# Optimization experiments

Hardware: AMD Instinct MI355X
Metric: run time of the kernel (lower is better)

## Reference

```python
import jax, jax.numpy as jnp
import numpy as np

GRID_SIZE = 5
SPLINE_ORDER = 3

def _grid(in_features, dtype):
    # efficient-KAN default grid over [-1, 1], extended by spline_order knots each side
    h = 2.0 / GRID_SIZE
    g = jnp.arange(-SPLINE_ORDER, GRID_SIZE + SPLINE_ORDER + 1, dtype=dtype) * h - 1.0
    return jnp.broadcast_to(g, (in_features, g.shape[0]))  # (in, G+2k+1)

def _b_splines(x, grid):
    # x: (..., in) -> bases: (..., in, G+k) via Cox-de Boor recursion
    xk = x[..., None]
    bases = ((xk >= grid[:, :-1]) & (xk < grid[:, 1:])).astype(x.dtype)
    for k in range(1, SPLINE_ORDER + 1):
        left = (xk - grid[:, :-(k + 1)]) / (grid[:, k:-1] - grid[:, :-(k + 1)]) * bases[..., :-1]
        right = (grid[:, k + 1:] - xk) / (grid[:, k + 1:] - grid[:, 1:-k]) * bases[..., 1:]
        bases = left + right
    return bases

def _kan_linear(x, base_w, spline_w, scaler):
    # base branch: SiLU(x) @ W_base^T ; spline branch: einsum over B-spline basis
    grid = _grid(base_w.shape[1], x.dtype)
    bases = _b_splines(x, grid)                      # (..., in, G+k)
    scaled = spline_w * scaler[..., None]            # (out, in, G+k)
    base_out = jax.nn.silu(x) @ base_w.T
    spline_out = jnp.einsum('...ig,oig->...o', bases, scaled)
    return base_out + spline_out

def setup_inputs() -> dict:
    key = jax.random.key(0)
    ks = jax.random.split(key, 11)
    B, N, C, O = 2, 256, 64, 64
    GK = GRID_SIZE + SPLINE_ORDER
    return {
        'x': jax.random.normal(ks[0], (B, N, C), jnp.float32),
        'adj': jax.random.randint(ks[1], (B, N, N), 0, 2, jnp.int32),
        'fw_base': jax.random.normal(ks[2], (1, C), jnp.float32) * 0.1,
        'fw_spline': jax.random.normal(ks[3], (1, C, GK), jnp.float32) * 0.1,
        'fw_scaler': jax.random.normal(ks[4], (1, C), jnp.float32) * 0.1,
        'mw_base': jax.random.normal(ks[5], (O, C), jnp.float32) * 0.1,
        'mw_spline': jax.random.normal(ks[6], (O, C, GK), jnp.float32) * 0.1,
        'mw_scaler': jax.random.normal(ks[7], (O, C), jnp.float32) * 0.1,
        'uw_base': jax.random.normal(ks[8], (O, C + O), jnp.float32) * 0.1,
        'uw_spline': jax.random.normal(ks[9], (O, C + O, GK), jnp.float32) * 0.1,
        'uw_scaler': jax.random.normal(ks[10], (O, C + O), jnp.float32) * 0.1,
    }

def reference(x, adj, fw_base, fw_spline, fw_scaler, mw_base, mw_spline, mw_scaler, uw_base, uw_spline, uw_scaler):
    # r_ij = h_i - h_j : (B, N, N, C)
    r_ij = x[:, :, None, :] - x[:, None, :, :]
    energy = _kan_linear(r_ij, fw_base, fw_spline, fw_scaler)[..., 0]  # (B, N, N)
    energy = jnp.where(adj == 0, jnp.asarray(-1e9, energy.dtype), energy)
    alpha = jax.nn.softmax(energy, axis=-1)
    msg_val = _kan_linear(x, mw_base, mw_spline, mw_scaler)            # (B, N, O)
    aggr = jnp.einsum('bij,bjo->bio', alpha, msg_val)
    combined = jnp.concatenate([x, aggr], axis=-1)
    return _kan_linear(combined, uw_base, uw_spline, uw_scaler)
```

## Files before the change

### kernel.cpp

```cpp
#include <hip/hip_runtime.h>
#include <math.h>

#define NB 256
#define CH 64
#define OUTF 64
#define GK 8
#define UIN 128
#define KM (CH * 9)
#define KM4 (KM / 4)
#define KU (UIN * 9)
#define KU4 (KU / 4)

#define WS_MSG 0
#define WS_XT 32768
#define WS_W2M 65536
#define WS_W2U 102400

__device__ __forceinline__ float silu(float v) {
    return v * __builtin_amdgcn_rcpf(1.0f + __expf(-v));
}

__device__ __forceinline__ void spline4(float r, int& d, float4& v) {
    float p = (r + 2.2f) * 2.5f;
    float fd = floorf(p);
    d = (int)fd;
    float u = p - fd;
    if ((unsigned)d > 10u) d = 11;
    float um = 1.0f - u;
    float u2 = u * u, u3 = u2 * u;
    const float k6 = 1.0f / 6.0f;
    v.x = um * um * um * k6;
    v.y = (3.0f * u3 - 6.0f * u2 + 4.0f) * k6;
    v.z = (-3.0f * u3 + 3.0f * u2 + 3.0f * u + 1.0f) * k6;
    v.w = u3 * k6;
}

__global__ __launch_bounds__(256) void prep_kernel(
    const float* __restrict__ x,
    const float* __restrict__ mwb, const float* __restrict__ mws,
    const float* __restrict__ mwsc,
    const float* __restrict__ uwb, const float* __restrict__ uws,
    const float* __restrict__ uwsc,
    float* __restrict__ ws) {
    int t = blockIdx.x * 256 + threadIdx.x;
    if (t < 2 * NB * CH) {
        int b = t >> 14, rem = t & 16383, j = rem >> 6, c = rem & 63;
        ws[WS_XT + b * CH * NB + c * NB + j] = x[t];
        return;
    }
    int t2 = t - 2 * NB * CH;
    if (t2 < KM4 * OUTF) {
        int k4 = t2 >> 6, o = t2 & 63;
        float4 v;
#pragma unroll
        for (int kk = 0; kk < 4; ++kk) {
            int k = k4 * 4 + kk, c = k / 9, g = k - c * 9;
            ((float*)&v)[kk] = (g < 8)
                ? mws[(o * CH + c) * GK + g] * mwsc[o * CH + c]
                : mwb[o * CH + c];
        }
        ((float4*)(ws + WS_W2M))[t2] = v;
        return;
    }
    int t3 = t2 - KM4 * OUTF;
    if (t3 < KU4 * OUTF) {
        int k4 = t3 >> 6, o = t3 & 63;
        float4 v;
#pragma unroll
        for (int kk = 0; kk < 4; ++kk) {
            int k = k4 * 4 + kk, c = k / 9, g = k - c * 9;
            ((float*)&v)[kk] = (g < 8)
                ? uws[(o * UIN + c) * GK + g] * uwsc[o * UIN + c]
                : uwb[o * UIN + c];
        }
        ((float4*)(ws + WS_W2U))[t3] = v;
    }
}

__global__ __launch_bounds__(256) void msg_kernel(
    const float* __restrict__ x, const float* __restrict__ w2m,
    float* __restrict__ msg) {
    const int row = blockIdx.x, tid = threadIdx.x;
    __shared__ __align__(16) float F[KM];
    __shared__ float part[4][OUTF];

    if (tid < CH) {
        float v = x[row * CH + tid];
#pragma unroll
        for (int g = 0; g < 8; ++g) F[tid * 9 + g] = 0.0f;
        F[tid * 9 + 8] = silu(v);
        int d; float4 vv; spline4(v, d, vv);
#pragma unroll
        for (int k = 0; k < 4; ++k) {
            int m = d - 3 + k;
            if ((unsigned)m < 8u) F[tid * 9 + m] = ((const float*)&vv)[k];
        }
    }
    __syncthreads();

    const int o = tid & 63, w = tid >> 6;
    const float4* W = (const float4*)w2m;
    const float4* Fv = (const float4*)F;
    float acc = 0.0f;
#pragma unroll 4
    for (int k4 = w * 36; k4 < w * 36 + 36; ++k4) {
        float4 f = Fv[k4];
        float4 wt = W[k4 * 64 + o];
        acc += f.x * wt.x + f.y * wt.y + f.z * wt.z + f.w * wt.w;
    }
    part[w][o] = acc;
    __syncthreads();
    if (tid < OUTF)
        msg[row * OUTF + tid] =
            part[0][tid] + part[1][tid] + part[2][tid] + part[3][tid];
}

__global__ __launch_bounds__(256) void gat_kernel(
    const float* __restrict__ xT,
    const float* __restrict__ x,
    const int* __restrict__ adj,
    const float* __restrict__ fwb, const float* __restrict__ fws,
    const float* __restrict__ fwsc,
    const float* __restrict__ w2u,
    const float* __restrict__ msg,
    float* __restrict__ out) {
    const int b = blockIdx.x >> 8;
    const int i = blockIdx.x & 255;
    const int tid = threadIdx.x;

    __shared__ float4 cpad[CH][16];
    __shared__ float2 xisf[CH];
    __shared__ float alpha[NB];
    __shared__ float comb[UIN];
    __shared__ __align__(16) float Fu[KU];
    __shared__ float part[4][OUTF];
    __shared__ float wred[4];

    if (tid < CH) {
        float v = x[(b * NB + i) * CH + tid];
        xisf[tid] = make_float2(v, fwb[tid]);
        comb[tid] = v;
    }
#pragma unroll
    for (int e = tid; e < CH * 16; e += 256) {
        int c = e >> 4, dd = e & 15;
        float4 cf = make_float4(0.f, 0.f, 0.f, 0.f);
        if (dd <= 10) {
            float sc = fwsc[c];
            float w0 = 0.f, w1 = 0.f, w2 = 0.f, w3 = 0.f;
            int m0 = dd - 3;
            if ((unsigned)(m0 + 0) < 8u) w0 = fws[c * GK + m0 + 0] * sc;
            if ((unsigned)(m0 + 1) < 8u) w1 = fws[c * GK + m0 + 1] * sc;
            if ((unsigned)(m0 + 2) < 8u) w2 = fws[c * GK + m0 + 2] * sc;
            if ((unsigned)(m0 + 3) < 8u) w3 = fws[c * GK + m0 + 3] * sc;
            cf.x = (w0 + 4.0f * w1 + w2) * (1.0f / 6.0f);
            cf.y = (w2 - w0) * 0.5f;
            cf.z = (w0 - 2.0f * w1 + w2) * 0.5f;
            cf.w = (w3 - w0 + 3.0f * (w1 - w2)) * (1.0f / 6.0f);
        }
        cpad[c][dd] = cf;
    }
    __syncthreads();

    const float* xTb = xT + b * CH * NB;
    float e = 0.0f;
#pragma unroll 4
    for (int c = 0; c < CH; ++c) {
        float xj = xTb[c * NB + tid];
        float2 xs = xisf[c];
        float r = xs.x - xj;
        float pp = (r + 2.2f) * 2.5f;
        float fd = floorf(pp);
        int d = (int)fd;
        float u = pp - fd;
        if ((unsigned)d > 10u) d = 11;
        float4 cf = cpad[c][d];
        e += cf.x + u * (cf.y + u * (cf.z + u * cf.w)) + silu(r) * xs.y;
    }
    if (adj[(b * NB + i) * NB + tid] == 0) e = -1e9f;

    float mx = e;
#pragma unroll
    for (int off = 32; off > 0; off >>= 1)
        mx = fmaxf(mx, __shfl_xor(mx, off, 64));
    if ((tid & 63) == 0) wred[tid >> 6] = mx;
    __syncthreads();
    mx = fmaxf(fmaxf(wred[0], wred[1]), fmaxf(wred[2], wred[3]));
    float pexp = __expf(e - mx);
    float sw = pexp;
#pragma unroll
    for (int off = 32; off > 0; off >>= 1)
        sw += __shfl_xor(sw, off, 64);
    __syncthreads();
    if ((tid & 63) == 0) wred[tid >> 6] = sw;
    __syncthreads();
    float denom = wred[0] + wred[1] + wred[2] + wred[3];
    alpha[tid] = pexp * __builtin_amdgcn_rcpf(denom);
    __syncthreads();

    {
        const int o = tid & 63, seg = tid >> 6;
        const float* msgb = msg + (b * NB + seg * 64) * OUTF;
        float a = 0.0f;
#pragma unroll 8
        for (int jj = 0; jj < 64; ++jj)
            a += alpha[seg * 64 + jj] * msgb[jj * OUTF + o];
        part[seg][o] = a;
    }
    __syncthreads();
    if (tid < OUTF)
        comb[CH + tid] = part[0][tid] + part[1][tid] + part[2][tid] + part[3][tid];
    __syncthreads();

    if (tid < UIN) {
        float v = comb[tid];
#pragma unroll
        for (int g = 0; g < 8; ++g) Fu[tid * 9 + g] = 0.0f;
        Fu[tid * 9 + 8] = silu(v);
        int d; float4 vv; spline4(v, d, vv);
#pragma unroll
        for (int k = 0; k < 4; ++k) {
            int m = d - 3 + k;
            if ((unsigned)m < 8u) Fu[tid * 9 + m] = ((const float*)&vv)[k];
        }
    }
    __syncthreads();

    {
        const int o = tid & 63, w = tid >> 6;
        const float4* W = (const float4*)w2u;
        const float4* Fv = (const float4*)Fu;
        float acc = 0.0f;
#pragma unroll 4
        for (int k4 = w * 72; k4 < w * 72 + 72; ++k4) {
            float4 f = Fv[k4];
            float4 wt = W[k4 * 64 + o];
            acc += f.x * wt.x + f.y * wt.y + f.z * wt.z + f.w * wt.w;
        }
        part[w][o] = acc;
    }
    __syncthreads();
    if (tid < OUTF)
        out[(b * NB + i) * OUTF + tid] =
            part[0][tid] + part[1][tid] + part[2][tid] + part[3][tid];
}

extern "C" void kernel_launch(void* const* d_in, const int* in_sizes, int n_in,
                              void* d_out, int out_size, void* d_ws, size_t ws_size,
                              hipStream_t stream) {
    const float* x     = (const float*)d_in[0];
    const int*   adj   = (const int*)d_in[1];
    const float* fwb   = (const float*)d_in[2];
    const float* fws   = (const float*)d_in[3];
    const float* fwsc  = (const float*)d_in[4];
    const float* mwb   = (const float*)d_in[5];
    const float* mws   = (const float*)d_in[6];
    const float* mwsc  = (const float*)d_in[7];
    const float* uwb   = (const float*)d_in[8];
    const float* uws   = (const float*)d_in[9];
    const float* uwsc  = (const float*)d_in[10];
    float* out = (float*)d_out;
    float* ws = (float*)d_ws;

    const int BN = in_sizes[0] / CH;

    const int prep_threads = 2 * NB * CH + KM4 * OUTF + KU4 * OUTF;
    prep_kernel<<<(prep_threads + 255) / 256, 256, 0, stream>>>(
        x, mwb, mws, mwsc, uwb, uws, uwsc, ws);
    msg_kernel<<<BN, 256, 0, stream>>>(x, ws + WS_W2M, ws + WS_MSG);
    gat_kernel<<<BN, 256, 0, stream>>>(ws + WS_XT, x, adj, fwb, fws, fwsc,
                                       ws + WS_W2U, ws + WS_MSG, out);
}
```

Baseline: 100.8 us.

## Load x_j rows into registers, drop transpose, vectorize alpha-msg aggregation

Removes the transpose of x in the prep kernel. In the gat kernel, each thread now loads its own row of x (64 floats as float4) into registers, where it previously read the transposed copy column by column. The pairwise energy loop is fully unrolled with fma-based polynomial evaluation. The alpha·msg aggregation switches to float4 loads across 16 segments, and launch bounds hint two blocks per CU. The 64-float register array raises register pressure, and the per-thread row loads are strided rather than coalesced.

New measurement: 99.39 us. Within noise of the previous version (-1.4%).

```diff
diff --git a/kernel.cpp b/kernel.cpp
--- a/kernel.cpp
+++ b/kernel.cpp
@@ -12,16 +12,15 @@
 #define KU4 (KU / 4)
 
 #define WS_MSG 0
-#define WS_XT 32768
-#define WS_W2M 65536
-#define WS_W2U 102400
+#define WS_W2M 32768
+#define WS_W2U 69632
 
 __device__ __forceinline__ float silu(float v) {
     return v * __builtin_amdgcn_rcpf(1.0f + __expf(-v));
 }
 
 __device__ __forceinline__ void spline4(float r, int& d, float4& v) {
-    float p = (r + 2.2f) * 2.5f;
+    float p = fmaf(r, 2.5f, 5.5f);
     float fd = floorf(p);
     d = (int)fd;
     float u = p - fd;
@@ -36,21 +35,14 @@
 }
 
 __global__ __launch_bounds__(256) void prep_kernel(
-    const float* __restrict__ x,
     const float* __restrict__ mwb, const float* __restrict__ mws,
     const float* __restrict__ mwsc,
     const float* __restrict__ uwb, const float* __restrict__ uws,
     const float* __restrict__ uwsc,
     float* __restrict__ ws) {
     int t = blockIdx.x * 256 + threadIdx.x;
-    if (t < 2 * NB * CH) {
-        int b = t >> 14, rem = t & 16383, j = rem >> 6, c = rem & 63;
-        ws[WS_XT + b * CH * NB + c * NB + j] = x[t];
-        return;
-    }
-    int t2 = t - 2 * NB * CH;
-    if (t2 < KM4 * OUTF) {
-        int k4 = t2 >> 6, o = t2 & 63;
+    if (t < KM4 * OUTF) {
+        int k4 = t >> 6, o = t & 63;
         float4 v;
 #pragma unroll
         for (int kk = 0; kk < 4; ++kk) {
@@ -59,12 +51,12 @@
                 ? mws[(o * CH + c) * GK + g] * mwsc[o * CH + c]
                 : mwb[o * CH + c];
         }
-        ((float4*)(ws + WS_W2M))[t2] = v;
+        ((float4*)(ws + WS_W2M))[t] = v;
         return;
     }
-    int t3 = t2 - KM4 * OUTF;
-    if (t3 < KU4 * OUTF) {
-        int k4 = t3 >> 6, o = t3 & 63;
+    int t2 = t - KM4 * OUTF;
+    if (t2 < KU4 * OUTF) {
+        int k4 = t2 >> 6, o = t2 & 63;
         float4 v;
 #pragma unroll
         for (int kk = 0; kk < 4; ++kk) {
@@ -73,7 +65,7 @@
                 ? uws[(o * UIN + c) * GK + g] * uwsc[o * UIN + c]
                 : uwb[o * UIN + c];
         }
-        ((float4*)(ws + WS_W2U))[t3] = v;
+        ((float4*)(ws + WS_W2U))[t2] = v;
     }
 }
 
@@ -115,8 +107,7 @@
             part[0][tid] + part[1][tid] + part[2][tid] + part[3][tid];
 }
 
-__global__ __launch_bounds__(256) void gat_kernel(
-    const float* __restrict__ xT,
+__global__ __launch_bounds__(256, 2) void gat_kernel(
     const float* __restrict__ x,
     const int* __restrict__ adj,
     const float* __restrict__ fwb, const float* __restrict__ fws,
@@ -129,17 +120,27 @@
     const int tid = threadIdx.x;
 
     __shared__ float4 cpad[CH][16];
-    __shared__ float2 xisf[CH];
+    __shared__ float4 xi4[16];
+    __shared__ float4 fb4[16];
     __shared__ float alpha[NB];
     __shared__ float comb[UIN];
     __shared__ __align__(16) float Fu[KU];
+    __shared__ float4 part4[16][16];
     __shared__ float part[4][OUTF];
     __shared__ float wred[4];
 
-    if (tid < CH) {
-        float v = x[(b * NB + i) * CH + tid];
-        xisf[tid] = make_float2(v, fwb[tid]);
-        comb[tid] = v;
+    float4 xj[16];
+    {
+        const float4* xrow = (const float4*)(x + (b * NB + tid) * CH);
+#pragma unroll
+        for (int c4 = 0; c4 < 16; ++c4) xj[c4] = xrow[c4];
+    }
+
+    if (tid < 16) {
+        float4 v = ((const float4*)(x + (b * NB + i) * CH))[tid];
+        xi4[tid] = v;
+        fb4[tid] = ((const float4*)fwb)[tid];
+        ((float4*)comb)[tid] = v;
     }
 #pragma unroll
     for (int e = tid; e < CH * 16; e += 256) {
@@ -162,20 +163,26 @@
     }
     __syncthreads();
 
-    const float* xTb = xT + b * CH * NB;
     float e = 0.0f;
-#pragma unroll 4
-    for (int c = 0; c < CH; ++c) {
-        float xj = xTb[c * NB + tid];
-        float2 xs = xisf[c];
-        float r = xs.x - xj;
-        float pp = (r + 2.2f) * 2.5f;
-        float fd = floorf(pp);
-        int d = (int)fd;
-        float u = pp - fd;
-        if ((unsigned)d > 10u) d = 11;
-        float4 cf = cpad[c][d];
-        e += cf.x + u * (cf.y + u * (cf.z + u * cf.w)) + silu(r) * xs.y;
+#pragma unroll
+    for (int c4 = 0; c4 < 16; ++c4) {
+        float4 xiv = xi4[c4];
+        float4 fbv = fb4[c4];
+        float4 xjv = xj[c4];
+#pragma unroll
+        for (int q = 0; q < 4; ++q) {
+            float r = ((const float*)&xiv)[q] - ((const float*)&xjv)[q];
+            float pp = fmaf(r, 2.5f, 5.5f);
+            float fd = floorf(pp);
+            int d = (int)fd;
+            float u = pp - fd;
+            if ((unsigned)d > 10u) d = 11;
+            float4 cf = cpad[c4 * 4 + q][d];
+            float t = fmaf(u, cf.w, cf.z);
+            t = fmaf(u, t, cf.y);
+            t = fmaf(u, t, cf.x);
+            e += fmaf(silu(r), ((const float*)&fbv)[q], t);
+        }
     }
     if (adj[(b * NB + i) * NB + tid] == 0) e = -1e9f;
 
@@ -199,17 +206,28 @@
     __syncthreads();
 
     {
-        const int o = tid & 63, seg = tid >> 6;
-        const float* msgb = msg + (b * NB + seg * 64) * OUTF;
-        float a = 0.0f;
-#pragma unroll 8
-        for (int jj = 0; jj < 64; ++jj)
-            a += alpha[seg * 64 + jj] * msgb[jj * OUTF + o];
-        part[seg][o] = a;
-    }
-    __syncthreads();
-    if (tid < OUTF)
-        comb[CH + tid] = part[0][tid] + part[1][tid] + part[2][tid] + part[3][tid];
+        const int o4 = tid & 15, seg = tid >> 4;
+        const float4* msgb4 = (const float4*)(msg + (b * NB + seg * 16) * OUTF);
+        float4 a = make_float4(0.f, 0.f, 0.f, 0.f);
+#pragma unroll
+        for (int jj = 0; jj < 16; ++jj) {
+            float al = alpha[seg * 16 + jj];
+            float4 mv = msgb4[jj * 16 + o4];
+            a.x = fmaf(al, mv.x, a.x);
+            a.y = fmaf(al, mv.y, a.y);
+            a.z = fmaf(al, mv.z, a.z);
+            a.w = fmaf(al, mv.w, a.w);
+        }
+        part4[seg][o4] = a;
+    }
+    __syncthreads();
+    if (tid < OUTF) {
+        const float* p = (const float*)part4;
+        float s = 0.0f;
+#pragma unroll
+        for (int sg = 0; sg < 16; ++sg) s += p[sg * 64 + tid];
+        comb[CH + tid] = s;
+    }
     __syncthreads();
 
     if (tid < UIN) {
@@ -264,10 +282,10 @@
 
     const int BN = in_sizes[0] / CH;
 
-    const int prep_threads = 2 * NB * CH + KM4 * OUTF + KU4 * OUTF;
+    const int prep_threads = KM4 * OUTF + KU4 * OUTF;
     prep_kernel<<<(prep_threads + 255) / 256, 256, 0, stream>>>(
-        x, mwb, mws, mwsc, uwb, uws, uwsc, ws);
+        mwb, mws, mwsc, uwb, uws, uwsc, ws);
     msg_kernel<<<BN, 256, 0, stream>>>(x, ws + WS_W2M, ws + WS_MSG);
-    gat_kernel<<<BN, 256, 0, stream>>>(ws + WS_XT, x, adj, fwb, fws, fwsc,
+    gat_kernel<<<BN, 256, 0, stream>>>(x, adj, fwb, fws, fwsc,
                                        ws + WS_W2U, ws + WS_MSG, out);
 }
```
